# Kernel tuning notes

Measured on AMD Instinct MI355X. Metric: run time of the kernel, lower is better.

## Reference

```python
import jax, jax.numpy as jnp
import numpy as np

DIM_LOC = 2
DIM_EMBED = 32
HID = 2 * DIM_EMBED  # 64, GRUCell input and hidden size
B, T = 65536, 24


def leaky(v):
    return jnp.where(v > 0, v, 0.2 * v)


def setup_inputs() -> dict:
    key = jax.random.key(0)
    ks = jax.random.split(key, 10)
    s = lambda fan: 1.0 / np.sqrt(fan)
    return {
        "x": jax.random.normal(ks[0], (B, T, DIM_LOC), dtype=jnp.float32),
        "W_loc": jax.random.uniform(ks[1], (DIM_LOC, DIM_EMBED), jnp.float32, -s(DIM_LOC), s(DIM_LOC)),
        "b_loc": jax.random.uniform(ks[2], (DIM_EMBED,), jnp.float32, -s(DIM_LOC), s(DIM_LOC)),
        "time_table": jax.random.normal(ks[3], (24, DIM_EMBED), dtype=jnp.float32),
        "W_ih": jax.random.uniform(ks[4], (3 * HID, HID), jnp.float32, -s(HID), s(HID)),
        "W_hh": jax.random.uniform(ks[5], (3 * HID, HID), jnp.float32, -s(HID), s(HID)),
        "b_ih": jax.random.uniform(ks[6], (3 * HID,), jnp.float32, -s(HID), s(HID)),
        "b_hh": jax.random.uniform(ks[7], (3 * HID,), jnp.float32, -s(HID), s(HID)),
        "W_pred": jax.random.uniform(ks[8], (HID, 1), jnp.float32, -s(HID), s(HID)),
        "b_pred": jax.random.uniform(ks[9], (1,), jnp.float32, -s(HID), s(HID)),
    }


def reference(x, W_loc, b_loc, time_table, W_ih, W_hh, b_ih, b_hh, W_pred, b_pred):
    Bn, Tn, _ = x.shape
    # location embedding + LeakyReLU(0.2): [B, T, 32]
    embed_x = leaky(jnp.einsum('btl,le->bte', x, W_loc) + b_loc)
    # time embedding + LeakyReLU(0.2) for t = 0..T-1: [T, 32]
    embed_t = leaky(time_table[:Tn])

    def gru_step(h, inp_t):
        ex_t, et_t = inp_t  # [B,32], [32]
        inp = jnp.concatenate(
            [ex_t, jnp.broadcast_to(et_t, (ex_t.shape[0], et_t.shape[0]))], axis=1)  # [B,64]
        gi = inp @ W_ih.T + b_ih   # [B, 192]
        gh = h @ W_hh.T + b_hh     # [B, 192]
        i_r, i_z, i_n = jnp.split(gi, 3, axis=1)
        h_r, h_z, h_n = jnp.split(gh, 3, axis=1)
        r = jax.nn.sigmoid(i_r + h_r)
        z = jax.nn.sigmoid(i_z + h_z)
        n = jnp.tanh(i_n + r * h_n)
        h_new = (1.0 - z) * n + z * h
        return h_new, None

    h0 = jnp.zeros((Bn, HID), dtype=x.dtype)
    xs = (jnp.transpose(embed_x, (1, 0, 2)), embed_t)  # time-major
    h_final, _ = jax.lax.scan(gru_step, h0, xs)
    out = jax.nn.sigmoid(h_final @ W_pred + b_pred)  # [B,1]
    return out.ravel()
```

## Files before the change

### kernel.cpp

```cpp
#include <hip/hip_runtime.h>
#include <hip/hip_bf16.h>

#define TN 24
#define HID 64
#define LOG2E 1.4426950408889634f

#define WS_GIC_F   0
#define WS_BHN_F   4608
#define WS_WLC_F   4672
#define WS_FRAG_B  19072

#define HHI_OFF  0
#define HLO_OFF  36864
#define WHH_OFF  73728
#define WI_OFF   98304
#define BHN_OFF  110592
#define WLC_OFF  110848
#define LDS_BYTES 111232

typedef __attribute__((ext_vector_type(8))) short bf16x8;
typedef __attribute__((ext_vector_type(4))) float f32x4;
typedef __attribute__((ext_vector_type(2))) float f32x2;

__device__ __forceinline__ ushort bf16rn(float f) {
    uint x = __float_as_uint(f);
    return (ushort)((x + 0x7fffu + ((x >> 16) & 1u)) >> 16);
}
__device__ __forceinline__ uint cvtpk_bf16(float lo, float hi) {
    uint r;
    asm("v_cvt_pk_bf16_f32 %0, %1, %2" : "=v"(r) : "v"(lo), "v"(hi));
    return r;
}
__device__ __forceinline__ float exp2p_(float x) {
    float r; asm("v_exp_f32 %0, %1" : "=v"(r) : "v"(x)); return r;
}
__device__ __forceinline__ float exp2n_(float x) {
    float r; asm("v_exp_f32 %0, -%1" : "=v"(r) : "v"(x)); return r;
}
__device__ __forceinline__ float sigm(float v) {
    return __builtin_amdgcn_rcpf(1.0f + __expf(-v));
}

extern "C" __global__ void __launch_bounds__(256)
traj_gru_pre(const float* __restrict__ Wloc, const float* __restrict__ bloc,
             const float* __restrict__ tt, const float* __restrict__ Wih,
             const float* __restrict__ Whh, const float* __restrict__ bih,
             const float* __restrict__ bhh, float* __restrict__ ws)
{
    const int b = blockIdx.x, tid = threadIdx.x;
    if (b < 36) {
        if (tid < 64) {
            const int er = tid & 15, cp = tid >> 4;
            const float* src;
            float s;
            if (b < 8) {
                int g = b >> 2, a = b & 3;
                src = Wih + (size_t)(g * 64 + a * 16 + er) * 64 + 8 * cp;
                s = LOG2E;
            } else if (b < 32) {
                int t = b - 8, g = t >> 3, r = t & 7, a = r >> 1, f = r & 1;
                src = Whh + (size_t)(g * 64 + a * 16 + er) * 64 + 32 * f + 8 * cp;
                s = (g == 2) ? 2.0f * LOG2E : LOG2E;
            } else {
                int a = b - 32;
                src = Wih + (size_t)(128 + a * 16 + er) * 64 + 8 * cp;
                s = 2.0f * LOG2E;
            }
            union { ushort u[8]; bf16x8 v; } fr;
            #pragma unroll
            for (int j = 0; j < 8; ++j) fr.u[j] = bf16rn(s * src[j]);
            *(bf16x8*)((char*)ws + WS_FRAG_B + ((size_t)b * 64 + tid) * 16) = fr.v;
        }
    } else if (b < 38) {
        const int base = (b - 36) * 2304;
        for (int i = tid; i < 2304; i += 256) {
            int idx = base + i, t = idx / 192, g = idx % 192;
            float acc = bih[g] + (g < 128 ? bhh[g] : 0.0f);
            const float* ttr = tt + t * 32;
            const float* wr  = Wih + g * 64 + 32;
            #pragma unroll
            for (int k = 0; k < 32; ++k) {
                float e = ttr[k];
                e = fmaxf(e, 0.2f * e);
                acc = fmaf(wr[k], e, acc);
            }
            ws[WS_GIC_F + idx] = acc * (g < 128 ? LOG2E : 2.0f * LOG2E);
        }
    } else {
        if (tid < 64) ws[WS_BHN_F + tid] = 2.0f * LOG2E * bhh[128 + tid];
        if (tid < 96) ws[WS_WLC_F + tid] = (tid < 64) ? Wloc[tid] : bloc[tid - 64];
    }
}

extern "C" __global__ void __launch_bounds__(512, 2)
traj_gru_mfma(const float* __restrict__ x, const float* __restrict__ ws,
              const float* __restrict__ Wpred, const float* __restrict__ bpred,
              float* __restrict__ out)
{
    extern __shared__ __align__(16) char L[];
    float*  Lf   = (float*)L;
    char*   whhS = L + WHH_OFF;
    char*   wiS  = L + WI_OFF;

    const int tid  = threadIdx.x;
    const int lane = tid & 63;
    const int wid  = tid >> 6;
    const int er   = lane & 15;
    const int cp   = lane >> 4;

    const char* fb = (const char*)ws + WS_FRAG_B;
    for (int i = tid; i < 36 * 64; i += 512) {
        int f = i >> 6, l = i & 63;
        bf16x8 v = *(const bf16x8*)(fb + (size_t)i * 16);
        char* dst;
        if (f < 8)       dst = wiS  + ((size_t)f * 64 + l) * 16;
        else if (f < 32) dst = whhS + ((size_t)(f - 8) * 64 + l) * 16;
        else             dst = wiS  + ((size_t)(f - 24) * 64 + l) * 16;
        *(bf16x8*)dst = v;
    }
    if (tid < 64) Lf[BHN_OFF / 4 + tid] = ws[WS_BHN_F + tid];
    if (tid < 96) Lf[WLC_OFF / 4 + tid] = ws[WS_WLC_F + tid];
    __syncthreads();

    const f32x2* wlc2 = (const f32x2*)(Lf + WLC_OFF / 4);
    ushort* Hhi = (ushort*)(L + HHI_OFF) + (size_t)(wid * 32) * 72;
    ushort* Hlo = (ushort*)(L + HLO_OFF) + (size_t)(wid * 32) * 72;

    f32x4 bhnR[4];
    #pragma unroll
    for (int a = 0; a < 4; ++a)
        bhnR[a] = *(const f32x4*)(Lf + BHN_OFF / 4 + a * 16 + 4 * cp);

    const int ego = (blockIdx.x * 8 + wid) * 32;
    const float* xr0 = x + (size_t)(ego + er) * (TN * 2);
    const float* xr1 = x + (size_t)(ego + 16 + er) * (TN * 2);

    f32x2 hold2[2][4][2];
    #pragma unroll
    for (int bf = 0; bf < 2; ++bf)
        #pragma unroll
        for (int a = 0; a < 4; ++a)
            #pragma unroll
            for (int p = 0; p < 2; ++p) hold2[bf][a][p] = (f32x2){0.0f, 0.0f};

    const f32x2 one2    = {1.0f, 1.0f};
    const f32x2 negtwo2 = {-2.0f, -2.0f};

    float2 xv0 = *(const float2*)(xr0);
    float2 xv1 = *(const float2*)(xr1);

    #pragma unroll 1
    for (int t = 0; t < TN; ++t) {
        const int tn = (t + 1 < TN) ? t + 1 : TN - 1;
        float2 xv0n = *(const float2*)(xr0 + tn * 2);
        float2 xv1n = *(const float2*)(xr1 + tn * 2);

        union { uint u[4]; bf16x8 v; } exf0, exf1;
        {
            f32x2 xx0 = {xv0.x, xv0.x}, yy0 = {xv0.y, xv0.y};
            f32x2 xx1 = {xv1.x, xv1.x}, yy1 = {xv1.y, xv1.y};
            #pragma unroll
            for (int jp = 0; jp < 4; ++jp) {
                int kp = 4 * cp + jp;
                f32x2 w1 = wlc2[kp], w2 = wlc2[16 + kp], bl = wlc2[32 + kp];
                f32x2 v0 = __builtin_elementwise_fma(xx0, w1,
                           __builtin_elementwise_fma(yy0, w2, bl));
                f32x2 v1 = __builtin_elementwise_fma(xx1, w1,
                           __builtin_elementwise_fma(yy1, w2, bl));
                exf0.u[jp] = cvtpk_bf16(fmaxf(v0.x, 0.2f * v0.x), fmaxf(v0.y, 0.2f * v0.y));
                exf1.u[jp] = cvtpk_bf16(fmaxf(v1.x, 0.2f * v1.x), fmaxf(v1.y, 0.2f * v1.y));
            }
        }

        const float* gt = ws + WS_GIC_F + t * 192;
        f32x4 gR[4], gZ[4], gNi[4];
        #pragma unroll
        for (int a = 0; a < 4; ++a) {
            gR[a]  = *(const f32x4*)(gt + a * 16 + 4 * cp);
            gZ[a]  = *(const f32x4*)(gt + 64 + a * 16 + 4 * cp);
            gNi[a] = *(const f32x4*)(gt + 128 + a * 16 + 4 * cp);
        }

        f32x4 accR[2][4], accZ[2][4], accNi[2][4], accNh[2][4];

        #pragma unroll
        for (int a = 0; a < 4; ++a) {
            bf16x8 wr = *(const bf16x8*)(wiS + ((size_t)a * 64 + lane) * 16);
            bf16x8 wz = *(const bf16x8*)(wiS + ((size_t)(4 + a) * 64 + lane) * 16);
            bf16x8 wn = *(const bf16x8*)(wiS + ((size_t)(8 + a) * 64 + lane) * 16);
            accR[0][a]  = __builtin_amdgcn_mfma_f32_16x16x32_bf16(wr, exf0.v, gR[a], 0, 0, 0);
            accR[1][a]  = __builtin_amdgcn_mfma_f32_16x16x32_bf16(wr, exf1.v, gR[a], 0, 0, 0);
            accZ[0][a]  = __builtin_amdgcn_mfma_f32_16x16x32_bf16(wz, exf0.v, gZ[a], 0, 0, 0);
            accZ[1][a]  = __builtin_amdgcn_mfma_f32_16x16x32_bf16(wz, exf1.v, gZ[a], 0, 0, 0);
            accNi[0][a] = __builtin_amdgcn_mfma_f32_16x16x32_bf16(wn, exf0.v, gNi[a], 0, 0, 0);
            accNi[1][a] = __builtin_amdgcn_mfma_f32_16x16x32_bf16(wn, exf1.v, gNi[a], 0, 0, 0);
        }

        if (t > 0) {
            bf16x8 hh0[2], hh1[2], hl0[2], hl1[2];
            #pragma unroll
            for (int bf = 0; bf < 2; ++bf) {
                const int row = (bf * 16 + er) * 72;
                hh0[bf] = *(const bf16x8*)&Hhi[row + 8 * cp];
                hh1[bf] = *(const bf16x8*)&Hhi[row + 32 + 8 * cp];
                hl0[bf] = *(const bf16x8*)&Hlo[row + 8 * cp];
                hl1[bf] = *(const bf16x8*)&Hlo[row + 32 + 8 * cp];
            }
            #pragma unroll
            for (int a = 0; a < 4; ++a) {
                bf16x8 wr0 = *(const bf16x8*)(whhS + ((size_t)(a * 2 + 0) * 64 + lane) * 16);
                bf16x8 wr1 = *(const bf16x8*)(whhS + ((size_t)(a * 2 + 1) * 64 + lane) * 16);
                accR[0][a] = __builtin_amdgcn_mfma_f32_16x16x32_bf16(wr0, hh0[0], accR[0][a], 0, 0, 0);
                accR[0][a] = __builtin_amdgcn_mfma_f32_16x16x32_bf16(wr1, hh1[0], accR[0][a], 0, 0, 0);
                accR[1][a] = __builtin_amdgcn_mfma_f32_16x16x32_bf16(wr0, hh0[1], accR[1][a], 0, 0, 0);
                accR[1][a] = __builtin_amdgcn_mfma_f32_16x16x32_bf16(wr1, hh1[1], accR[1][a], 0, 0, 0);
                bf16x8 wz0 = *(const bf16x8*)(whhS + ((size_t)(8 + a * 2 + 0) * 64 + lane) * 16);
                bf16x8 wz1 = *(const bf16x8*)(whhS + ((size_t)(8 + a * 2 + 1) * 64 + lane) * 16);
                accZ[0][a] = __builtin_amdgcn_mfma_f32_16x16x32_bf16(wz0, hh0[0], accZ[0][a], 0, 0, 0);
                accZ[0][a] = __builtin_amdgcn_mfma_f32_16x16x32_bf16(wz1, hh1[0], accZ[0][a], 0, 0, 0);
                accZ[1][a] = __builtin_amdgcn_mfma_f32_16x16x32_bf16(wz0, hh0[1], accZ[1][a], 0, 0, 0);
                accZ[1][a] = __builtin_amdgcn_mfma_f32_16x16x32_bf16(wz1, hh1[1], accZ[1][a], 0, 0, 0);
                bf16x8 wn0 = *(const bf16x8*)(whhS + ((size_t)(16 + a * 2 + 0) * 64 + lane) * 16);
                bf16x8 wn1 = *(const bf16x8*)(whhS + ((size_t)(16 + a * 2 + 1) * 64 + lane) * 16);
                accNh[0][a] = __builtin_amdgcn_mfma_f32_16x16x32_bf16(wn0, hh0[0], bhnR[a], 0, 0, 0);
                accNh[0][a] = __builtin_amdgcn_mfma_f32_16x16x32_bf16(wn1, hh1[0], accNh[0][a], 0, 0, 0);
                accNh[0][a] = __builtin_amdgcn_mfma_f32_16x16x32_bf16(wn0, hl0[0], accNh[0][a], 0, 0, 0);
                accNh[0][a] = __builtin_amdgcn_mfma_f32_16x16x32_bf16(wn1, hl1[0], accNh[0][a], 0, 0, 0);
                accNh[1][a] = __builtin_amdgcn_mfma_f32_16x16x32_bf16(wn0, hh0[1], bhnR[a], 0, 0, 0);
                accNh[1][a] = __builtin_amdgcn_mfma_f32_16x16x32_bf16(wn1, hh1[1], accNh[1][a], 0, 0, 0);
                accNh[1][a] = __builtin_amdgcn_mfma_f32_16x16x32_bf16(wn0, hl0[1], accNh[1][a], 0, 0, 0);
                accNh[1][a] = __builtin_amdgcn_mfma_f32_16x16x32_bf16(wn1, hl1[1], accNh[1][a], 0, 0, 0);
            }
        } else {
            #pragma unroll
            for (int bf = 0; bf < 2; ++bf)
                #pragma unroll
                for (int a = 0; a < 4; ++a) accNh[bf][a] = bhnR[a];
        }

        #pragma unroll
        for (int bf = 0; bf < 2; ++bf) {
            const int row = (bf * 16 + er) * 72;
            #pragma unroll
            for (int a = 0; a < 4; ++a) {
                uint hiw[2], low[2];
                #pragma unroll
                for (int p = 0; p < 2; ++p) {
                    f32x2 aR  = {accR[bf][a][2 * p],  accR[bf][a][2 * p + 1]};
                    f32x2 aZ  = {accZ[bf][a][2 * p],  accZ[bf][a][2 * p + 1]};
                    f32x2 aNi = {accNi[bf][a][2 * p], accNi[bf][a][2 * p + 1]};
                    f32x2 aNh = {accNh[bf][a][2 * p], accNh[bf][a][2 * p + 1]};
                    f32x2 eR = {exp2n_(aR.x), exp2n_(aR.y)};
                    f32x2 eZ = {exp2n_(aZ.x), exp2n_(aZ.y)};
                    f32x2 dR = eR + one2;
                    f32x2 dZ = eZ + one2;
                    f32x2 r  = {__builtin_amdgcn_rcpf(dR.x), __builtin_amdgcn_rcpf(dR.y)};
                    f32x2 z  = {__builtin_amdgcn_rcpf(dZ.x), __builtin_amdgcn_rcpf(dZ.y)};
                    f32x2 np = __builtin_elementwise_fma(r, aNh, aNi);
                    f32x2 e2 = {exp2p_(np.x), exp2p_(np.y)};
                    f32x2 d2 = e2 + one2;
                    f32x2 rc = {__builtin_amdgcn_rcpf(d2.x), __builtin_amdgcn_rcpf(d2.y)};
                    f32x2 n  = __builtin_elementwise_fma(rc, negtwo2, one2);
                    f32x2 hm = hold2[bf][a][p] - n;
                    f32x2 h  = __builtin_elementwise_fma(z, hm, n);
                    hold2[bf][a][p] = h;
                    uint whi = cvtpk_bf16(h.x, h.y);
                    f32x2 hh = {__uint_as_float(whi << 16), __uint_as_float(whi & 0xffff0000u)};
                    f32x2 lo = h - hh;
                    hiw[p] = whi;
                    low[p] = cvtpk_bf16(lo.x, lo.y);
                }
                uint2 whiv = {hiw[0], hiw[1]};
                uint2 wlov = {low[0], low[1]};
                *(uint2*)&Hhi[row + 16 * a + 4 * cp] = whiv;
                *(uint2*)&Hlo[row + 16 * a + 4 * cp] = wlov;
            }
        }

        xv0 = xv0n;
        xv1 = xv1n;
    }

    float p0 = 0.0f, p1 = 0.0f;
    #pragma unroll
    for (int a = 0; a < 4; ++a) {
        f32x4 wp = *(const f32x4*)(Wpred + 16 * a + 4 * cp);
        #pragma unroll
        for (int p = 0; p < 2; ++p) {
            p0 = fmaf(hold2[0][a][p].x, wp[2 * p], p0);
            p0 = fmaf(hold2[0][a][p].y, wp[2 * p + 1], p0);
            p1 = fmaf(hold2[1][a][p].x, wp[2 * p], p1);
            p1 = fmaf(hold2[1][a][p].y, wp[2 * p + 1], p1);
        }
    }
    p0 += __shfl_xor(p0, 16);  p0 += __shfl_xor(p0, 32);
    p1 += __shfl_xor(p1, 16);  p1 += __shfl_xor(p1, 32);
    if (cp == 0) {
        float bp = bpred[0];
        out[ego + er]      = sigm(p0 + bp);
        out[ego + 16 + er] = sigm(p1 + bp);
    }
}

extern "C" void kernel_launch(void* const* d_in, const int* in_sizes, int n_in,
                              void* d_out, int out_size, void* d_ws, size_t ws_size,
                              hipStream_t stream) {
    const float* x     = (const float*)d_in[0];
    const float* Wloc  = (const float*)d_in[1];
    const float* bloc  = (const float*)d_in[2];
    const float* tt    = (const float*)d_in[3];
    const float* Wih   = (const float*)d_in[4];
    const float* Whh   = (const float*)d_in[5];
    const float* bih   = (const float*)d_in[6];
    const float* bhh   = (const float*)d_in[7];
    const float* Wpred = (const float*)d_in[8];
    const float* bpred = (const float*)d_in[9];
    float* out = (float*)d_out;
    float* ws  = (float*)d_ws;

    (void)hipFuncSetAttribute((const void*)traj_gru_mfma,
                              hipFuncAttributeMaxDynamicSharedMemorySize, LDS_BYTES);

    hipLaunchKernelGGL(traj_gru_pre, dim3(39), dim3(256), 0, stream,
                       Wloc, bloc, tt, Wih, Whh, bih, bhh, ws);
    hipLaunchKernelGGL(traj_gru_mfma, dim3(256), dim3(512), LDS_BYTES, stream,
                       x, ws, Wpred, bpred, out);
}
```

Before: 114.2 us.

## Split each GRU batch tile's hidden units across a wave pair with block barriers

Each group of 32 sequences is now handled by a pair of waves, each computing half of the 64 hidden units, instead of one wave computing all of them. The hidden-state LDS tiles are shared per pair, so two __syncthreads per timestep order the reads of h against its writes, and the final prediction dot product is combined through a small LDS partial buffer. LDS per block is roughly halved, launch bounds go to 4 blocks per CU and the grid doubles, aiming for more waves in flight and more latency hiding. The cost is two block-wide barriers per step and redundant per-wave embedding and x work.

New measurement: 254.5 us. 2.23x slower.

```diff
diff --git a/kernel.cpp b/kernel.cpp
--- a/kernel.cpp
+++ b/kernel.cpp
@@ -10,13 +10,14 @@
 #define WS_WLC_F   4672
 #define WS_FRAG_B  19072
 
-#define HHI_OFF  0
-#define HLO_OFF  36864
-#define WHH_OFF  73728
-#define WI_OFF   98304
-#define BHN_OFF  110592
-#define WLC_OFF  110848
-#define LDS_BYTES 111232
+#define HHI_OFF   0
+#define HLO_OFF   18432
+#define WHH_OFF   36864
+#define WI_OFF    61440
+#define BHN_OFF   73728
+#define WLC_OFF   73984
+#define PARTS_OFF 74368
+#define LDS_BYTES 75392
 
 typedef __attribute__((ext_vector_type(8))) short bf16x8;
 typedef __attribute__((ext_vector_type(4))) float f32x4;
@@ -92,7 +93,7 @@
     }
 }
 
-extern "C" __global__ void __launch_bounds__(512, 2)
+extern "C" __global__ void __launch_bounds__(512, 4)
 traj_gru_mfma(const float* __restrict__ x, const float* __restrict__ ws,
               const float* __restrict__ Wpred, const float* __restrict__ bpred,
               float* __restrict__ out)
@@ -105,6 +106,8 @@
     const int tid  = threadIdx.x;
     const int lane = tid & 63;
     const int wid  = tid >> 6;
+    const int pair = wid >> 1;
+    const int half = wid & 1;
     const int er   = lane & 15;
     const int cp   = lane >> 4;
 
@@ -123,23 +126,23 @@
     __syncthreads();
 
     const f32x2* wlc2 = (const f32x2*)(Lf + WLC_OFF / 4);
-    ushort* Hhi = (ushort*)(L + HHI_OFF) + (size_t)(wid * 32) * 72;
-    ushort* Hlo = (ushort*)(L + HLO_OFF) + (size_t)(wid * 32) * 72;
-
-    f32x4 bhnR[4];
+    ushort* Hhi = (ushort*)(L + HHI_OFF) + (size_t)(pair * 32) * 72;
+    ushort* Hlo = (ushort*)(L + HLO_OFF) + (size_t)(pair * 32) * 72;
+
+    f32x4 bhnR[2];
     #pragma unroll
-    for (int a = 0; a < 4; ++a)
-        bhnR[a] = *(const f32x4*)(Lf + BHN_OFF / 4 + a * 16 + 4 * cp);
-
-    const int ego = (blockIdx.x * 8 + wid) * 32;
+    for (int a = 0; a < 2; ++a)
+        bhnR[a] = *(const f32x4*)(Lf + BHN_OFF / 4 + (half * 2 + a) * 16 + 4 * cp);
+
+    const int ego = (blockIdx.x * 4 + pair) * 32;
     const float* xr0 = x + (size_t)(ego + er) * (TN * 2);
     const float* xr1 = x + (size_t)(ego + 16 + er) * (TN * 2);
 
-    f32x2 hold2[2][4][2];
+    f32x2 hold2[2][2][2];
     #pragma unroll
     for (int bf = 0; bf < 2; ++bf)
         #pragma unroll
-        for (int a = 0; a < 4; ++a)
+        for (int a = 0; a < 2; ++a)
             #pragma unroll
             for (int p = 0; p < 2; ++p) hold2[bf][a][p] = (f32x2){0.0f, 0.0f};
 
@@ -173,21 +176,23 @@
         }
 
         const float* gt = ws + WS_GIC_F + t * 192;
-        f32x4 gR[4], gZ[4], gNi[4];
-        #pragma unroll
-        for (int a = 0; a < 4; ++a) {
-            gR[a]  = *(const f32x4*)(gt + a * 16 + 4 * cp);
-            gZ[a]  = *(const f32x4*)(gt + 64 + a * 16 + 4 * cp);
-            gNi[a] = *(const f32x4*)(gt + 128 + a * 16 + 4 * cp);
-        }
-
-        f32x4 accR[2][4], accZ[2][4], accNi[2][4], accNh[2][4];
-
-        #pragma unroll
-        for (int a = 0; a < 4; ++a) {
-            bf16x8 wr = *(const bf16x8*)(wiS + ((size_t)a * 64 + lane) * 16);
-            bf16x8 wz = *(const bf16x8*)(wiS + ((size_t)(4 + a) * 64 + lane) * 16);
-            bf16x8 wn = *(const bf16x8*)(wiS + ((size_t)(8 + a) * 64 + lane) * 16);
+        f32x4 gR[2], gZ[2], gNi[2];
+        #pragma unroll
+        for (int a = 0; a < 2; ++a) {
+            const int ao = half * 2 + a;
+            gR[a]  = *(const f32x4*)(gt + ao * 16 + 4 * cp);
+            gZ[a]  = *(const f32x4*)(gt + 64 + ao * 16 + 4 * cp);
+            gNi[a] = *(const f32x4*)(gt + 128 + ao * 16 + 4 * cp);
+        }
+
+        f32x4 accR[2][2], accZ[2][2], accNi[2][2], accNh[2][2];
+
+        #pragma unroll
+        for (int a = 0; a < 2; ++a) {
+            const int ao = half * 2 + a;
+            bf16x8 wr = *(const bf16x8*)(wiS + ((size_t)ao * 64 + lane) * 16);
+            bf16x8 wz = *(const bf16x8*)(wiS + ((size_t)(4 + ao) * 64 + lane) * 16);
+            bf16x8 wn = *(const bf16x8*)(wiS + ((size_t)(8 + ao) * 64 + lane) * 16);
             accR[0][a]  = __builtin_amdgcn_mfma_f32_16x16x32_bf16(wr, exf0.v, gR[a], 0, 0, 0);
             accR[1][a]  = __builtin_amdgcn_mfma_f32_16x16x32_bf16(wr, exf1.v, gR[a], 0, 0, 0);
             accZ[0][a]  = __builtin_amdgcn_mfma_f32_16x16x32_bf16(wz, exf0.v, gZ[a], 0, 0, 0);
@@ -197,52 +202,47 @@
         }
 
         if (t > 0) {
-            bf16x8 hh0[2], hh1[2], hl0[2], hl1[2];
             #pragma unroll
             for (int bf = 0; bf < 2; ++bf) {
                 const int row = (bf * 16 + er) * 72;
-                hh0[bf] = *(const bf16x8*)&Hhi[row + 8 * cp];
-                hh1[bf] = *(const bf16x8*)&Hhi[row + 32 + 8 * cp];
-                hl0[bf] = *(const bf16x8*)&Hlo[row + 8 * cp];
-                hl1[bf] = *(const bf16x8*)&Hlo[row + 32 + 8 * cp];
-            }
-            #pragma unroll
-            for (int a = 0; a < 4; ++a) {
-                bf16x8 wr0 = *(const bf16x8*)(whhS + ((size_t)(a * 2 + 0) * 64 + lane) * 16);
-                bf16x8 wr1 = *(const bf16x8*)(whhS + ((size_t)(a * 2 + 1) * 64 + lane) * 16);
-                accR[0][a] = __builtin_amdgcn_mfma_f32_16x16x32_bf16(wr0, hh0[0], accR[0][a], 0, 0, 0);
-                accR[0][a] = __builtin_amdgcn_mfma_f32_16x16x32_bf16(wr1, hh1[0], accR[0][a], 0, 0, 0);
-                accR[1][a] = __builtin_amdgcn_mfma_f32_16x16x32_bf16(wr0, hh0[1], accR[1][a], 0, 0, 0);
-                accR[1][a] = __builtin_amdgcn_mfma_f32_16x16x32_bf16(wr1, hh1[1], accR[1][a], 0, 0, 0);
-                bf16x8 wz0 = *(const bf16x8*)(whhS + ((size_t)(8 + a * 2 + 0) * 64 + lane) * 16);
-                bf16x8 wz1 = *(const bf16x8*)(whhS + ((size_t)(8 + a * 2 + 1) * 64 + lane) * 16);
-                accZ[0][a] = __builtin_amdgcn_mfma_f32_16x16x32_bf16(wz0, hh0[0], accZ[0][a], 0, 0, 0);
-                accZ[0][a] = __builtin_amdgcn_mfma_f32_16x16x32_bf16(wz1, hh1[0], accZ[0][a], 0, 0, 0);
-                accZ[1][a] = __builtin_amdgcn_mfma_f32_16x16x32_bf16(wz0, hh0[1], accZ[1][a], 0, 0, 0);
-                accZ[1][a] = __builtin_amdgcn_mfma_f32_16x16x32_bf16(wz1, hh1[1], accZ[1][a], 0, 0, 0);
-                bf16x8 wn0 = *(const bf16x8*)(whhS + ((size_t)(16 + a * 2 + 0) * 64 + lane) * 16);
-                bf16x8 wn1 = *(const bf16x8*)(whhS + ((size_t)(16 + a * 2 + 1) * 64 + lane) * 16);
-                accNh[0][a] = __builtin_amdgcn_mfma_f32_16x16x32_bf16(wn0, hh0[0], bhnR[a], 0, 0, 0);
-                accNh[0][a] = __builtin_amdgcn_mfma_f32_16x16x32_bf16(wn1, hh1[0], accNh[0][a], 0, 0, 0);
-                accNh[0][a] = __builtin_amdgcn_mfma_f32_16x16x32_bf16(wn0, hl0[0], accNh[0][a], 0, 0, 0);
-                accNh[0][a] = __builtin_amdgcn_mfma_f32_16x16x32_bf16(wn1, hl1[0], accNh[0][a], 0, 0, 0);
-                accNh[1][a] = __builtin_amdgcn_mfma_f32_16x16x32_bf16(wn0, hh0[1], bhnR[a], 0, 0, 0);
-                accNh[1][a] = __builtin_amdgcn_mfma_f32_16x16x32_bf16(wn1, hh1[1], accNh[1][a], 0, 0, 0);
-                accNh[1][a] = __builtin_amdgcn_mfma_f32_16x16x32_bf16(wn0, hl0[1], accNh[1][a], 0, 0, 0);
-                accNh[1][a] = __builtin_amdgcn_mfma_f32_16x16x32_bf16(wn1, hl1[1], accNh[1][a], 0, 0, 0);
+                bf16x8 hh0 = *(const bf16x8*)&Hhi[row + 8 * cp];
+                bf16x8 hh1 = *(const bf16x8*)&Hhi[row + 32 + 8 * cp];
+                bf16x8 hl0 = *(const bf16x8*)&Hlo[row + 8 * cp];
+                bf16x8 hl1 = *(const bf16x8*)&Hlo[row + 32 + 8 * cp];
+                #pragma unroll
+                for (int a = 0; a < 2; ++a) {
+                    const int ao = half * 2 + a;
+                    bf16x8 wr0 = *(const bf16x8*)(whhS + ((size_t)(ao * 2 + 0) * 64 + lane) * 16);
+                    bf16x8 wr1 = *(const bf16x8*)(whhS + ((size_t)(ao * 2 + 1) * 64 + lane) * 16);
+                    accR[bf][a] = __builtin_amdgcn_mfma_f32_16x16x32_bf16(wr0, hh0, accR[bf][a], 0, 0, 0);
+                    accR[bf][a] = __builtin_amdgcn_mfma_f32_16x16x32_bf16(wr1, hh1, accR[bf][a], 0, 0, 0);
+                    bf16x8 wz0 = *(const bf16x8*)(whhS + ((size_t)(8 + ao * 2 + 0) * 64 + lane) * 16);
+                    bf16x8 wz1 = *(const bf16x8*)(whhS + ((size_t)(8 + ao * 2 + 1) * 64 + lane) * 16);
+                    accZ[bf][a] = __builtin_amdgcn_mfma_f32_16x16x32_bf16(wz0, hh0, accZ[bf][a], 0, 0, 0);
+                    accZ[bf][a] = __builtin_amdgcn_mfma_f32_16x16x32_bf16(wz1, hh1, accZ[bf][a], 0, 0, 0);
+                    bf16x8 wn0 = *(const bf16x8*)(whhS + ((size_t)(16 + ao * 2 + 0) * 64 + lane) * 16);
+                    bf16x8 wn1 = *(const bf16x8*)(whhS + ((size_t)(16 + ao * 2 + 1) * 64 + lane) * 16);
+                    accNh[bf][a] = __builtin_amdgcn_mfma_f32_16x16x32_bf16(wn0, hh0, bhnR[a], 0, 0, 0);
+                    accNh[bf][a] = __builtin_amdgcn_mfma_f32_16x16x32_bf16(wn1, hh1, accNh[bf][a], 0, 0, 0);
+                    accNh[bf][a] = __builtin_amdgcn_mfma_f32_16x16x32_bf16(wn0, hl0, accNh[bf][a], 0, 0, 0);
+                    accNh[bf][a] = __builtin_amdgcn_mfma_f32_16x16x32_bf16(wn1, hl1, accNh[bf][a], 0, 0, 0);
+                }
             }
         } else {
             #pragma unroll
             for (int bf = 0; bf < 2; ++bf)
                 #pragma unroll
-                for (int a = 0; a < 4; ++a) accNh[bf][a] = bhnR[a];
-        }
+                for (int a = 0; a < 2; ++a) accNh[bf][a] = bhnR[a];
+        }
+
+        __syncthreads();
 
         #pragma unroll
         for (int bf = 0; bf < 2; ++bf) {
             const int row = (bf * 16 + er) * 72;
             #pragma unroll
-            for (int a = 0; a < 4; ++a) {
+            for (int a = 0; a < 2; ++a) {
+                const int ao = half * 2 + a;
                 uint hiw[2], low[2];
                 #pragma unroll
                 for (int p = 0; p < 2; ++p) {
@@ -272,10 +272,12 @@
                 }
                 uint2 whiv = {hiw[0], hiw[1]};
                 uint2 wlov = {low[0], low[1]};
-                *(uint2*)&Hhi[row + 16 * a + 4 * cp] = whiv;
-                *(uint2*)&Hlo[row + 16 * a + 4 * cp] = wlov;
-            }
-        }
+                *(uint2*)&Hhi[row + 16 * ao + 4 * cp] = whiv;
+                *(uint2*)&Hlo[row + 16 * ao + 4 * cp] = wlov;
+            }
+        }
+
+        __syncthreads();
 
         xv0 = xv0n;
         xv1 = xv1n;
@@ -283,8 +285,9 @@
 
     float p0 = 0.0f, p1 = 0.0f;
     #pragma unroll
-    for (int a = 0; a < 4; ++a) {
-        f32x4 wp = *(const f32x4*)(Wpred + 16 * a + 4 * cp);
+    for (int a = 0; a < 2; ++a) {
+        const int ao = half * 2 + a;
+        f32x4 wp = *(const f32x4*)(Wpred + 16 * ao + 4 * cp);
         #pragma unroll
         for (int p = 0; p < 2; ++p) {
             p0 = fmaf(hold2[0][a][p].x, wp[2 * p], p0);
@@ -295,10 +298,19 @@
     }
     p0 += __shfl_xor(p0, 16);  p0 += __shfl_xor(p0, 32);
     p1 += __shfl_xor(p1, 16);  p1 += __shfl_xor(p1, 32);
+
+    float* parts = Lf + PARTS_OFF / 4;
     if (cp == 0) {
+        parts[(pair * 2 + half) * 32 + er]      = p0;
+        parts[(pair * 2 + half) * 32 + 16 + er] = p1;
+    }
+    __syncthreads();
+    if (half == 0 && cp == 0) {
         float bp = bpred[0];
-        out[ego + er]      = sigm(p0 + bp);
-        out[ego + 16 + er] = sigm(p1 + bp);
+        float q0 = parts[(pair * 2 + 1) * 32 + er];
+        float q1 = parts[(pair * 2 + 1) * 32 + 16 + er];
+        out[ego + er]      = sigm(p0 + q0 + bp);
+        out[ego + 16 + er] = sigm(p1 + q1 + bp);
     }
 }
 
@@ -323,6 +335,6 @@
 
     hipLaunchKernelGGL(traj_gru_pre, dim3(39), dim3(256), 0, stream,
                        Wloc, bloc, tt, Wih, Whh, bih, bhh, ws);
-    hipLaunchKernelGGL(traj_gru_mfma, dim3(256), dim3(512), LDS_BYTES, stream,
+    hipLaunchKernelGGL(traj_gru_mfma, dim3(512), dim3(512), LDS_BYTES, stream,
                        x, ws, Wpred, bpred, out);
 }
```
